# Performance work log

Hardware: AMD Instinct MI355X
Metric: run time of the kernel (lower is better)

The kernel has to match this reference:

```python
import jax, jax.numpy as jnp
import numpy as np

N = 50000   # nodes
E = 800000  # edges
F = 128     # feat_dim
LN_EPS = 1e-5


def setup_inputs() -> dict:
    key = jax.random.key(0)
    ks = jax.random.split(key, 16)

    def lin(k, fan_in, shape):
        # roughly kaiming-uniform-like scale; exact init is irrelevant for correctness
        return jax.random.normal(k, shape, jnp.float32) * (1.0 / np.sqrt(fan_in))

    inp = {
        "x": jax.random.normal(ks[0], (N, F), jnp.float32),
        "pos": jax.random.normal(ks[1], (N, 3), jnp.float32),
        "edge_index": jax.random.randint(ks[2], (2, E), 0, N, jnp.int64),
        # edge_mlp: Linear(2F+1 -> F), SiLU, Linear(F -> F)
        "ew1": lin(ks[3], 2 * F + 1, (2 * F + 1, F)),
        "eb1": jnp.zeros((F,), jnp.float32),
        "ew2": lin(ks[4], F, (F, F)),
        "eb2": jnp.zeros((F,), jnp.float32),
        # node_mlp: Linear(F -> F), SiLU, Linear(F -> F)
        "nw1": lin(ks[5], F, (F, F)),
        "nb1": jnp.zeros((F,), jnp.float32),
        "nw2": lin(ks[6], F, (F, F)),
        "nb2": jnp.zeros((F,), jnp.float32),
        # coord_mlp: Linear(F -> 1), Tanh
        "cw": lin(ks[7], F, (F, 1)),
        "cb": jnp.zeros((1,), jnp.float32),
        # LayerNorm(F)
        "gamma": jnp.ones((F,), jnp.float32),
        "beta": jnp.zeros((F,), jnp.float32),
    }
    return inp


def reference(x, pos, edge_index, ew1, eb1, ew2, eb2, nw1, nb1, nw2, nb2, cw, cb, gamma, beta):
    row, col = edge_index[0], edge_index[1]

    diff = pos[row] - pos[col]                              # [E, 3]
    dist2 = jnp.sum(diff * diff, axis=1, keepdims=True)     # [E, 1]
    edge_feat = jnp.concatenate([x[row], x[col], dist2], axis=1)  # [E, 2F+1]

    # edge MLP (dropout p=0 -> identity in eval)
    msg = jax.nn.silu(edge_feat @ ew1 + eb1) @ ew2 + eb2    # [E, F]

    # scatter-add messages to source nodes
    agg = jax.ops.segment_sum(msg, row, num_segments=N)     # [N, F]

    # node MLP + residual + LayerNorm
    upd = jax.nn.silu(agg @ nw1 + nb1) @ nw2 + nb2          # [N, F]
    pre = x + upd
    mean = jnp.mean(pre, axis=-1, keepdims=True)
    var = jnp.mean(jnp.square(pre - mean), axis=-1, keepdims=True)
    x_out = gamma * (pre - mean) * jax.lax.rsqrt(var + LN_EPS) + beta

    # coordinate update
    scale = jnp.tanh(msg @ cw + cb)                         # [E, 1]
    delta = jax.ops.segment_sum(scale * diff, row, num_segments=N)  # [N, 3]
    pos_out = pos + delta
    return (x_out, pos_out)
```

## Files before the change

### kernel.cpp

```cpp
#include <hip/hip_runtime.h>
#include <math.h>

#define NN 50000
#define EE 800000
#define FF 128

constexpr float LN_EPS = 1e-5f;
constexpr int NC = (NN + 255) / 256;

typedef float  f32x4  __attribute__((ext_vector_type(4)));
typedef short  s16x8  __attribute__((ext_vector_type(8)));

__device__ __forceinline__ float silu_f(float v) {
    return v / (1.f + __expf(-v));
}

__device__ __forceinline__ unsigned short f2bf(float f) {
    union { float f; unsigned u; } cv; cv.f = f;
    unsigned u = cv.u;
    u += 0x7fffu + ((u >> 16) & 1u);
    return (unsigned short)(u >> 16);
}

__device__ __forceinline__ float bf2f(unsigned short u) {
    union { unsigned u; float f; } cv; cv.u = ((unsigned)u) << 16;
    return cv.f;
}

__global__ __launch_bounds__(256) void convert_x_kernel(
    const float* __restrict__ x, unsigned short* __restrict__ xb)
{
    int i = (blockIdx.x * 256 + threadIdx.x) * 8;
    float4 a = *(const float4*)&x[i];
    float4 b = *(const float4*)&x[i + 4];
    s16x8 o;
    o[0] = (short)f2bf(a.x); o[1] = (short)f2bf(a.y);
    o[2] = (short)f2bf(a.z); o[3] = (short)f2bf(a.w);
    o[4] = (short)f2bf(b.x); o[5] = (short)f2bf(b.y);
    o[6] = (short)f2bf(b.z); o[7] = (short)f2bf(b.w);
    *(s16x8*)&xb[i] = o;
}

__global__ __launch_bounds__(256) void transpose_w_kernel(
    const float* __restrict__ ew1, const float* __restrict__ ew2,
    const float* __restrict__ nw1, const float* __restrict__ nw2,
    unsigned short* __restrict__ ew1T, unsigned short* __restrict__ ew2T,
    unsigned short* __restrict__ nw1T, unsigned short* __restrict__ nw2T)
{
    int o = blockIdx.x * 256 + threadIdx.x;
    if (o < 32768) {
        int n = o >> 8, k = o & 255;
        ew1T[o] = f2bf(ew1[k * FF + n]);
    } else if (o < 49152) {
        int o2 = o - 32768; int n = o2 >> 7, k = o2 & 127;
        ew2T[o2] = f2bf(ew2[k * FF + n]);
    } else if (o < 65536) {
        int o2 = o - 49152; int n = o2 >> 7, k = o2 & 127;
        nw1T[o2] = f2bf(nw1[k * FF + n]);
    } else {
        int o2 = o - 65536; int n = o2 >> 7, k = o2 & 127;
        nw2T[o2] = f2bf(nw2[k * FF + n]);
    }
}

__global__ __launch_bounds__(256) void hist_kernel(
    const int* __restrict__ ei, int* __restrict__ cnt)
{
    int e = blockIdx.x * 256 + threadIdx.x;
    if (e < EE) atomicAdd(&cnt[ei[e]], 1);
}

__global__ __launch_bounds__(256) void chunk_sum_kernel(
    const int* __restrict__ cnt, int* __restrict__ chunkSum)
{
    __shared__ int s[256];
    int t = threadIdx.x;
    int idx = blockIdx.x * 256 + t;
    s[t] = (idx < NN) ? cnt[idx] : 0;
    __syncthreads();
    for (int off = 128; off > 0; off >>= 1) {
        if (t < off) s[t] += s[t + off];
        __syncthreads();
    }
    if (t == 0) chunkSum[blockIdx.x] = s[0];
}

__global__ __launch_bounds__(256) void scan_chunks_kernel(
    const int* __restrict__ chunkSum, int* __restrict__ chunkOff)
{
    __shared__ int s[256];
    int t = threadIdx.x;
    int v = (t < NC) ? chunkSum[t] : 0;
    s[t] = v;
    __syncthreads();
    for (int off = 1; off < 256; off <<= 1) {
        int u = (t >= off) ? s[t - off] : 0;
        __syncthreads();
        s[t] += u;
        __syncthreads();
    }
    if (t < NC) chunkOff[t] = s[t] - v;
}

__global__ __launch_bounds__(256) void scan_kernel(
    const int* __restrict__ cnt, const int* __restrict__ chunkOff,
    int* __restrict__ offs, int* __restrict__ rowStart)
{
    __shared__ int s[256];
    int t = threadIdx.x;
    int idx = blockIdx.x * 256 + t;
    int v = (idx < NN) ? cnt[idx] : 0;
    s[t] = v;
    __syncthreads();
    for (int off = 1; off < 256; off <<= 1) {
        int u = (t >= off) ? s[t - off] : 0;
        __syncthreads();
        s[t] += u;
        __syncthreads();
    }
    if (idx < NN) {
        int st = chunkOff[blockIdx.x] + s[t] - v;
        offs[idx] = st;
        rowStart[idx] = st;
    }
}

__global__ __launch_bounds__(256) void scatter_idx_kernel(
    const int* __restrict__ ei, int* __restrict__ offs,
    int* __restrict__ sRow, int* __restrict__ sCol)
{
    int e = blockIdx.x * 256 + threadIdx.x;
    if (e < EE) {
        int r = ei[e], c = ei[EE + e];
        int p = atomicAdd(&offs[r], 1);
        sRow[p] = r;
        sCol[p] = c;
    }
}

constexpr int EPB   = 64;
constexpr int NTILE = EE / EPB;
constexpr int XAS   = 264;
constexpr int H1S   = 136;

__global__ __launch_bounds__(512, 4) void edgeA_kernel(
    const unsigned short* __restrict__ xb, const float* __restrict__ pos,
    const int* __restrict__ sRow, const int* __restrict__ sCol,
    const unsigned short* __restrict__ ew1T, const float* __restrict__ ew1,
    const float* __restrict__ eb1,
    const unsigned short* __restrict__ ew2T, const float* __restrict__ eb2,
    const float* __restrict__ cw,  const float* __restrict__ cb,
    unsigned short* __restrict__ msgb, float* __restrict__ sSg)
{
    __shared__ float dist2S[EPB];
    __shared__ float sPart[8][EPB];
    __shared__ __align__(16) unsigned short xa  [EPB * XAS];
    __shared__ __align__(16) unsigned short h1  [EPB * H1S];
    __shared__ __align__(16) unsigned short msgL[EPB * H1S];

    const int t   = threadIdx.x;
    const int w   = t >> 6;
    const int l   = t & 63;
    const int l15 = l & 15;
    const int q8  = l >> 4;
    const int n   = w * 16 + l15;

    s16x8 B1[8], B2[4];
    #pragma unroll
    for (int ko = 0; ko < 8; ++ko)
        B1[ko] = *(const s16x8*)(ew1T + (size_t)n * 256 + ko * 32 + q8 * 8);
    #pragma unroll
    for (int ko = 0; ko < 4; ++ko)
        B2[ko] = *(const s16x8*)(ew2T + (size_t)n * 128 + ko * 32 + q8 * 8);
    const float w256 = ew1[256 * FF + n];
    const float b1   = eb1[n];
    const float b2   = eb2[n];
    const float cwc  = cw[n];
    const float cb0  = cb[0];

    const int q   = t & 31;
    const int eB  = t >> 5;
    const int ksel = (q & 15) * 8;
    const int* idxBase = (q < 16) ? sRow : sCol;

    int   nidx[4];
    s16x8 ag[4];
    {
        int e0 = blockIdx.x * EPB;
        #pragma unroll
        for (int i = 0; i < 4; ++i) nidx[i] = idxBase[e0 + eB + 16 * i];
        #pragma unroll
        for (int i = 0; i < 4; ++i) ag[i] = *(const s16x8*)(xb + (size_t)nidx[i] * FF + ksel);
    }

    for (int tile = blockIdx.x; tile < NTILE; tile += gridDim.x) {
        const int e0 = tile * EPB;

        #pragma unroll
        for (int i = 0; i < 4; ++i)
            *(s16x8*)(xa + (eB + 16 * i) * XAS + q * 8) = ag[i];
        if (t < EPB) {
            int r = sRow[e0 + t];
            int c = sCol[e0 + t];
            float dx = pos[r*3+0] - pos[c*3+0];
            float dy = pos[r*3+1] - pos[c*3+1];
            float dz = pos[r*3+2] - pos[c*3+2];
            dist2S[t] = dx*dx + dy*dy + dz*dz;
        }
        __syncthreads();

        {
            int tn  = tile + gridDim.x;
            int e0n = (tn < NTILE) ? tn * EPB : 0;
            #pragma unroll
            for (int i = 0; i < 4; ++i) nidx[i] = idxBase[e0n + eB + 16 * i];
            #pragma unroll
            for (int i = 0; i < 4; ++i) ag[i] = *(const s16x8*)(xb + (size_t)nidx[i] * FF + ksel);
        }

        f32x4 acc[4] = {};
        #pragma unroll
        for (int mt = 0; mt < 4; ++mt) {
            const unsigned short* ar = xa + (mt * 16 + l15) * XAS + q8 * 8;
            #pragma unroll
            for (int ko = 0; ko < 8; ++ko) {
                s16x8 a = *(const s16x8*)(ar + ko * 32);
                acc[mt] = __builtin_amdgcn_mfma_f32_16x16x32_bf16(a, B1[ko], acc[mt], 0, 0, 0);
            }
        }

        #pragma unroll
        for (int mt = 0; mt < 4; ++mt) {
            #pragma unroll
            for (int r = 0; r < 4; ++r) {
                int e = mt * 16 + q8 * 4 + r;
                float v = acc[mt][r] + dist2S[e] * w256 + b1;
                h1[e * H1S + n] = f2bf(silu_f(v));
            }
        }
        __syncthreads();

        f32x4 acc2[4] = {};
        #pragma unroll
        for (int mt = 0; mt < 4; ++mt) {
            const unsigned short* hr = h1 + (mt * 16 + l15) * H1S + q8 * 8;
            #pragma unroll
            for (int ko = 0; ko < 4; ++ko) {
                s16x8 a = *(const s16x8*)(hr + ko * 32);
                acc2[mt] = __builtin_amdgcn_mfma_f32_16x16x32_bf16(a, B2[ko], acc2[mt], 0, 0, 0);
            }
        }

        #pragma unroll
        for (int mt = 0; mt < 4; ++mt) {
            #pragma unroll
            for (int r = 0; r < 4; ++r) {
                float m = acc2[mt][r] + b2;
                float p = m * cwc;
                p += __shfl_xor(p, 1);
                p += __shfl_xor(p, 2);
                p += __shfl_xor(p, 4);
                p += __shfl_xor(p, 8);
                int e = mt * 16 + q8 * 4 + r;
                if (l15 == 0) sPart[w][e] = p;
                msgL[e * H1S + n] = f2bf(m);
            }
        }
        __syncthreads();

        if (t < EPB) {
            float p = 0.f;
            #pragma unroll
            for (int ww = 0; ww < 8; ++ww) p += sPart[ww][t];
            sSg[e0 + t] = tanhf(p + cb0);
        }

        #pragma unroll
        for (int i = 0; i < 2; ++i) {
            int idx = i * 512 + t;
            int e   = idx >> 4;
            int c   = idx & 15;
            *(s16x8*)&msgb[(size_t)(e0 + e) * FF + c * 8] =
                *(const s16x8*)&msgL[e * H1S + c * 8];
        }
    }
}

constexpr int NPB  = 16;
constexpr int ABS  = 136;

__global__ __launch_bounds__(128) void nodeB_kernel(
    const float* __restrict__ x, const float* __restrict__ pos,
    const unsigned short* __restrict__ msgb, const float* __restrict__ sSg,
    const int* __restrict__ sCol, const int* __restrict__ rowStart,
    const unsigned short* __restrict__ nw1T, const float* __restrict__ nb1,
    const unsigned short* __restrict__ nw2T, const float* __restrict__ nb2,
    const float* __restrict__ gamma, const float* __restrict__ beta,
    float* __restrict__ xout, float* __restrict__ posout)
{
    __shared__ __align__(16) unsigned short aB [NPB * ABS];
    __shared__ __align__(16) unsigned short h1B[NPB * ABS];
    __shared__ float sRedS[2][NPB];
    __shared__ float sRedQ[2][NPB];

    const int t   = threadIdx.x;
    const int w   = t >> 6;
    const int l   = t & 63;
    const int l15 = l & 15;
    const int q8  = l >> 4;

    const int n0 = blockIdx.x * NPB;

    for (int e = 0; e < NPB; ++e) {
        int nn = n0 + e;
        int p0 = rowStart[nn];
        int p1 = (nn == NN - 1) ? EE : rowStart[nn + 1];
        float s0 = 0.f, s1 = 0.f, s2 = 0.f, s3 = 0.f;
        int p = p0;
        for (; p + 4 <= p1; p += 4) {
            s0 += bf2f(msgb[(size_t)(p    ) * FF + t]);
            s1 += bf2f(msgb[(size_t)(p + 1) * FF + t]);
            s2 += bf2f(msgb[(size_t)(p + 2) * FF + t]);
            s3 += bf2f(msgb[(size_t)(p + 3) * FF + t]);
        }
        for (; p < p1; ++p) s0 += bf2f(msgb[(size_t)p * FF + t]);
        aB[e * ABS + t] = f2bf((s0 + s1) + (s2 + s3));
    }

    if (t < NPB * 3) {
        int e = t / 3, d = t % 3;
        int nn = n0 + e;
        int p0 = rowStart[nn];
        int p1 = (nn == NN - 1) ? EE : rowStart[nn + 1];
        float pn = pos[nn * 3 + d];
        float sum = 0.f;
        for (int p = p0; p < p1; ++p) {
            int c = sCol[p];
            sum += sSg[p] * (pn - pos[c * 3 + d]);
        }
        posout[nn * 3 + d] = pn + sum;
    }
    __syncthreads();

    int ncol[4];
    #pragma unroll
    for (int tt = 0; tt < 4; ++tt) ncol[tt] = w * 64 + tt * 16 + l15;

    f32x4 acc[4] = {};
    {
        const unsigned short* ar = aB + l15 * ABS + q8 * 8;
        #pragma unroll
        for (int ko = 0; ko < 4; ++ko) {
            s16x8 a = *(const s16x8*)(ar + ko * 32);
            #pragma unroll
            for (int tt = 0; tt < 4; ++tt) {
                s16x8 b = *(const s16x8*)(nw1T + (size_t)ncol[tt] * 128 + ko * 32 + q8 * 8);
                acc[tt] = __builtin_amdgcn_mfma_f32_16x16x32_bf16(a, b, acc[tt], 0, 0, 0);
            }
        }
    }
    #pragma unroll
    for (int tt = 0; tt < 4; ++tt) {
        float bb = nb1[ncol[tt]];
        #pragma unroll
        for (int r = 0; r < 4; ++r) {
            int e = q8 * 4 + r;
            h1B[e * ABS + ncol[tt]] = f2bf(silu_f(acc[tt][r] + bb));
        }
    }
    __syncthreads();

    f32x4 acc2[4] = {};
    {
        const unsigned short* hr = h1B + l15 * ABS + q8 * 8;
        #pragma unroll
        for (int ko = 0; ko < 4; ++ko) {
            s16x8 a = *(const s16x8*)(hr + ko * 32);
            #pragma unroll
            for (int tt = 0; tt < 4; ++tt) {
                s16x8 b = *(const s16x8*)(nw2T + (size_t)ncol[tt] * 128 + ko * 32 + q8 * 8);
                acc2[tt] = __builtin_amdgcn_mfma_f32_16x16x32_bf16(a, b, acc2[tt], 0, 0, 0);
            }
        }
    }

    float pre[4][4];
    #pragma unroll
    for (int tt = 0; tt < 4; ++tt) {
        float bb = nb2[ncol[tt]];
        #pragma unroll
        for (int r = 0; r < 4; ++r) {
            int e = q8 * 4 + r;
            pre[tt][r] = x[(size_t)(n0 + e) * FF + ncol[tt]] + acc2[tt][r] + bb;
        }
    }
    #pragma unroll
    for (int r = 0; r < 4; ++r) {
        float s = 0.f, sq = 0.f;
        #pragma unroll
        for (int tt = 0; tt < 4; ++tt) {
            s  += pre[tt][r];
            sq += pre[tt][r] * pre[tt][r];
        }
        s  += __shfl_xor(s, 1);  sq += __shfl_xor(sq, 1);
        s  += __shfl_xor(s, 2);  sq += __shfl_xor(sq, 2);
        s  += __shfl_xor(s, 4);  sq += __shfl_xor(sq, 4);
        s  += __shfl_xor(s, 8);  sq += __shfl_xor(sq, 8);
        if (l15 == 0) {
            int e = q8 * 4 + r;
            sRedS[w][e] = s;
            sRedQ[w][e] = sq;
        }
    }
    __syncthreads();

    #pragma unroll
    for (int tt = 0; tt < 4; ++tt) {
        float g = gamma[ncol[tt]], bb = beta[ncol[tt]];
        #pragma unroll
        for (int r = 0; r < 4; ++r) {
            int e = q8 * 4 + r;
            float mean = (sRedS[0][e] + sRedS[1][e]) * (1.f / FF);
            float m2   = (sRedQ[0][e] + sRedQ[1][e]) * (1.f / FF);
            float var  = m2 - mean * mean;
            float xo   = g * (pre[tt][r] - mean) * rsqrtf(var + LN_EPS) + bb;
            xout[(size_t)(n0 + e) * FF + ncol[tt]] = xo;
        }
    }
}

extern "C" void kernel_launch(void* const* d_in, const int* in_sizes, int n_in,
                              void* d_out, int out_size, void* d_ws, size_t ws_size,
                              hipStream_t stream) {
    const float* x    = (const float*)d_in[0];
    const float* pos  = (const float*)d_in[1];
    const int*   ei   = (const int*)  d_in[2];
    const float* ew1  = (const float*)d_in[3];
    const float* eb1  = (const float*)d_in[4];
    const float* ew2  = (const float*)d_in[5];
    const float* eb2  = (const float*)d_in[6];
    const float* nw1  = (const float*)d_in[7];
    const float* nb1  = (const float*)d_in[8];
    const float* nw2  = (const float*)d_in[9];
    const float* nb2  = (const float*)d_in[10];
    const float* cw   = (const float*)d_in[11];
    const float* cb   = (const float*)d_in[12];
    const float* gam  = (const float*)d_in[13];
    const float* bet  = (const float*)d_in[14];

    float* out    = (float*)d_out;
    float* xout   = out;
    float* posout = out + (size_t)NN * FF;

    auto align256 = [](size_t v) { return (v + 255) & ~(size_t)255; };
    char* ws = (char*)d_ws;

    size_t CNT_B   = align256((size_t)NN * 4);
    size_t OFFS_B  = align256((size_t)NN * 4);
    size_t RST_B   = align256((size_t)NN * 4);
    size_t CHNK_B  = align256((size_t)NC * 4 * 2);
    size_t SROW_B  = align256((size_t)EE * 4);
    size_t XB_B    = align256((size_t)NN * FF * 2);
    size_t EW1T_B  = align256((size_t)128 * 256 * 2);
    size_t WT_B    = align256((size_t)128 * 128 * 2);
    size_t MSGB_B  = align256((size_t)EE * FF * 2);

    size_t o = 0;
    int* cnt       = (int*)(ws + o);  o += CNT_B;
    int* offs      = (int*)(ws + o);  o += OFFS_B;
    int* rowStart  = (int*)(ws + o);  o += RST_B;
    int* chunkSum  = (int*)(ws + o);
    int* chunkOff  = chunkSum + NC;   o += CHNK_B;
    int* sRow      = (int*)(ws + o);  o += SROW_B;
    int* sCol      = (int*)(ws + o);  o += SROW_B;
    unsigned short* xb   = (unsigned short*)(ws + o);  o += XB_B;
    unsigned short* ew1T = (unsigned short*)(ws + o);  o += EW1T_B;
    unsigned short* ew2T = (unsigned short*)(ws + o);  o += WT_B;
    unsigned short* nw1T = (unsigned short*)(ws + o);  o += WT_B;
    unsigned short* nw2T = (unsigned short*)(ws + o);  o += WT_B;
    unsigned short* msgb = (unsigned short*)(ws + o);  o += MSGB_B;
    float*          sSg  = (float*)(ws + o);

    hipMemsetAsync(cnt, 0, CNT_B, stream);

    convert_x_kernel<<<(NN * FF / 8) / 256, 256, 0, stream>>>(x, xb);
    transpose_w_kernel<<<(32768 + 3 * 16384) / 256, 256, 0, stream>>>(
        ew1, ew2, nw1, nw2, ew1T, ew2T, nw1T, nw2T);

    hist_kernel<<<(EE + 255) / 256, 256, 0, stream>>>(ei, cnt);
    chunk_sum_kernel<<<NC, 256, 0, stream>>>(cnt, chunkSum);
    scan_chunks_kernel<<<1, 256, 0, stream>>>(chunkSum, chunkOff);
    scan_kernel<<<NC, 256, 0, stream>>>(cnt, chunkOff, offs, rowStart);
    scatter_idx_kernel<<<(EE + 255) / 256, 256, 0, stream>>>(ei, offs, sRow, sCol);

    edgeA_kernel<<<2048, 512, 0, stream>>>(
        xb, pos, sRow, sCol, ew1T, ew1, eb1, ew2T, eb2, cw, cb, msgb, sSg);

    nodeB_kernel<<<NN / NPB, 128, 0, stream>>>(
        x, pos, msgb, sSg, sCol, rowStart,
        nw1T, nb1, nw2T, nb2, gam, bet, xout, posout);
}
```

Before: 527.6 us.

## Widen node kernel to 512 threads with vectorized per-wave segment aggregation

The node kernel grows from 128 to 512 threads per block. Each of the 8 waves now aggregates two nodes' message rows using 16-byte bf16 vector loads, with four edges in flight per wave and a shuffle reduction, replacing the serial per-node loop that loaded one element per thread. The node MLPs are re-split so each wave owns one 16-column MFMA tile instead of four, and the LayerNorm partial sums are reduced across 8 waves. This aims to raise memory-level parallelism in the gather-heavy aggregation, at the cost of larger blocks and more cross-wave reduction.

```diff
diff --git a/kernel.cpp b/kernel.cpp
--- a/kernel.cpp
+++ b/kernel.cpp
@@ -286,10 +286,10 @@
     }
 }
 
-constexpr int NPB  = 16;
-constexpr int ABS  = 136;
-
-__global__ __launch_bounds__(128) void nodeB_kernel(
+constexpr int NPB = 16;
+constexpr int ABS = 136;
+
+__global__ __launch_bounds__(512) void nodeB_kernel(
     const float* __restrict__ x, const float* __restrict__ pos,
     const unsigned short* __restrict__ msgb, const float* __restrict__ sSg,
     const int* __restrict__ sCol, const int* __restrict__ rowStart,
@@ -300,31 +300,51 @@
 {
     __shared__ __align__(16) unsigned short aB [NPB * ABS];
     __shared__ __align__(16) unsigned short h1B[NPB * ABS];
-    __shared__ float sRedS[2][NPB];
-    __shared__ float sRedQ[2][NPB];
+    __shared__ float sRedS[8][NPB];
+    __shared__ float sRedQ[8][NPB];
 
     const int t   = threadIdx.x;
     const int w   = t >> 6;
     const int l   = t & 63;
     const int l15 = l & 15;
     const int q8  = l >> 4;
-
-    const int n0 = blockIdx.x * NPB;
-
-    for (int e = 0; e < NPB; ++e) {
+    const int n0  = blockIdx.x * NPB;
+    const int n   = w * 16 + l15;
+
+    #pragma unroll
+    for (int s = 0; s < 2; ++s) {
+        int e  = 2 * w + s;
         int nn = n0 + e;
         int p0 = rowStart[nn];
         int p1 = (nn == NN - 1) ? EE : rowStart[nn + 1];
-        float s0 = 0.f, s1 = 0.f, s2 = 0.f, s3 = 0.f;
-        int p = p0;
-        for (; p + 4 <= p1; p += 4) {
-            s0 += bf2f(msgb[(size_t)(p    ) * FF + t]);
-            s1 += bf2f(msgb[(size_t)(p + 1) * FF + t]);
-            s2 += bf2f(msgb[(size_t)(p + 2) * FF + t]);
-            s3 += bf2f(msgb[(size_t)(p + 3) * FF + t]);
-        }
-        for (; p < p1; ++p) s0 += bf2f(msgb[(size_t)p * FF + t]);
-        aB[e * ABS + t] = f2bf((s0 + s1) + (s2 + s3));
+        float a0=0.f,a1=0.f,a2=0.f,a3=0.f,a4=0.f,a5=0.f,a6=0.f,a7=0.f;
+        for (int p = p0 + q8; p < p1; p += 4) {
+            s16x8 v = *(const s16x8*)(msgb + (size_t)p * FF + l15 * 8);
+            a0 += bf2f((unsigned short)v[0]);
+            a1 += bf2f((unsigned short)v[1]);
+            a2 += bf2f((unsigned short)v[2]);
+            a3 += bf2f((unsigned short)v[3]);
+            a4 += bf2f((unsigned short)v[4]);
+            a5 += bf2f((unsigned short)v[5]);
+            a6 += bf2f((unsigned short)v[6]);
+            a7 += bf2f((unsigned short)v[7]);
+        }
+        a0 += __shfl_xor(a0,16); a1 += __shfl_xor(a1,16);
+        a2 += __shfl_xor(a2,16); a3 += __shfl_xor(a3,16);
+        a4 += __shfl_xor(a4,16); a5 += __shfl_xor(a5,16);
+        a6 += __shfl_xor(a6,16); a7 += __shfl_xor(a7,16);
+        a0 += __shfl_xor(a0,32); a1 += __shfl_xor(a1,32);
+        a2 += __shfl_xor(a2,32); a3 += __shfl_xor(a3,32);
+        a4 += __shfl_xor(a4,32); a5 += __shfl_xor(a5,32);
+        a6 += __shfl_xor(a6,32); a7 += __shfl_xor(a7,32);
+        if (q8 == 0) {
+            s16x8 o;
+            o[0]=(short)f2bf(a0); o[1]=(short)f2bf(a1);
+            o[2]=(short)f2bf(a2); o[3]=(short)f2bf(a3);
+            o[4]=(short)f2bf(a4); o[5]=(short)f2bf(a5);
+            o[6]=(short)f2bf(a6); o[7]=(short)f2bf(a7);
+            *(s16x8*)(aB + e * ABS + l15 * 8) = o;
+        }
     }
 
     if (t < NPB * 3) {
@@ -342,70 +362,53 @@
     }
     __syncthreads();
 
-    int ncol[4];
-    #pragma unroll
-    for (int tt = 0; tt < 4; ++tt) ncol[tt] = w * 64 + tt * 16 + l15;
-
-    f32x4 acc[4] = {};
+    f32x4 acc = {};
     {
         const unsigned short* ar = aB + l15 * ABS + q8 * 8;
         #pragma unroll
         for (int ko = 0; ko < 4; ++ko) {
             s16x8 a = *(const s16x8*)(ar + ko * 32);
-            #pragma unroll
-            for (int tt = 0; tt < 4; ++tt) {
-                s16x8 b = *(const s16x8*)(nw1T + (size_t)ncol[tt] * 128 + ko * 32 + q8 * 8);
-                acc[tt] = __builtin_amdgcn_mfma_f32_16x16x32_bf16(a, b, acc[tt], 0, 0, 0);
-            }
-        }
-    }
-    #pragma unroll
-    for (int tt = 0; tt < 4; ++tt) {
-        float bb = nb1[ncol[tt]];
+            s16x8 b = *(const s16x8*)(nw1T + (size_t)n * 128 + ko * 32 + q8 * 8);
+            acc = __builtin_amdgcn_mfma_f32_16x16x32_bf16(a, b, acc, 0, 0, 0);
+        }
+    }
+    {
+        float bb = nb1[n];
         #pragma unroll
         for (int r = 0; r < 4; ++r) {
             int e = q8 * 4 + r;
-            h1B[e * ABS + ncol[tt]] = f2bf(silu_f(acc[tt][r] + bb));
+            h1B[e * ABS + n] = f2bf(silu_f(acc[r] + bb));
         }
     }
     __syncthreads();
 
-    f32x4 acc2[4] = {};
+    f32x4 acc2 = {};
     {
         const unsigned short* hr = h1B + l15 * ABS + q8 * 8;
         #pragma unroll
         for (int ko = 0; ko < 4; ++ko) {
             s16x8 a = *(const s16x8*)(hr + ko * 32);
-            #pragma unroll
-            for (int tt = 0; tt < 4; ++tt) {
-                s16x8 b = *(const s16x8*)(nw2T + (size_t)ncol[tt] * 128 + ko * 32 + q8 * 8);
-                acc2[tt] = __builtin_amdgcn_mfma_f32_16x16x32_bf16(a, b, acc2[tt], 0, 0, 0);
-            }
-        }
-    }
-
-    float pre[4][4];
-    #pragma unroll
-    for (int tt = 0; tt < 4; ++tt) {
-        float bb = nb2[ncol[tt]];
+            s16x8 b = *(const s16x8*)(nw2T + (size_t)n * 128 + ko * 32 + q8 * 8);
+            acc2 = __builtin_amdgcn_mfma_f32_16x16x32_bf16(a, b, acc2, 0, 0, 0);
+        }
+    }
+
+    float pre[4];
+    {
+        float bb = nb2[n];
         #pragma unroll
         for (int r = 0; r < 4; ++r) {
             int e = q8 * 4 + r;
-            pre[tt][r] = x[(size_t)(n0 + e) * FF + ncol[tt]] + acc2[tt][r] + bb;
+            pre[r] = x[(size_t)(n0 + e) * FF + n] + acc2[r] + bb;
         }
     }
     #pragma unroll
     for (int r = 0; r < 4; ++r) {
-        float s = 0.f, sq = 0.f;
-        #pragma unroll
-        for (int tt = 0; tt < 4; ++tt) {
-            s  += pre[tt][r];
-            sq += pre[tt][r] * pre[tt][r];
-        }
-        s  += __shfl_xor(s, 1);  sq += __shfl_xor(sq, 1);
-        s  += __shfl_xor(s, 2);  sq += __shfl_xor(sq, 2);
-        s  += __shfl_xor(s, 4);  sq += __shfl_xor(sq, 4);
-        s  += __shfl_xor(s, 8);  sq += __shfl_xor(sq, 8);
+        float s = pre[r], sq = pre[r] * pre[r];
+        s += __shfl_xor(s, 1);  sq += __shfl_xor(sq, 1);
+        s += __shfl_xor(s, 2);  sq += __shfl_xor(sq, 2);
+        s += __shfl_xor(s, 4);  sq += __shfl_xor(sq, 4);
+        s += __shfl_xor(s, 8);  sq += __shfl_xor(sq, 8);
         if (l15 == 0) {
             int e = q8 * 4 + r;
             sRedS[w][e] = s;
@@ -414,17 +417,18 @@
     }
     __syncthreads();
 
-    #pragma unroll
-    for (int tt = 0; tt < 4; ++tt) {
-        float g = gamma[ncol[tt]], bb = beta[ncol[tt]];
+    {
+        float g = gamma[n], bt = beta[n];
         #pragma unroll
         for (int r = 0; r < 4; ++r) {
             int e = q8 * 4 + r;
-            float mean = (sRedS[0][e] + sRedS[1][e]) * (1.f / FF);
-            float m2   = (sRedQ[0][e] + sRedQ[1][e]) * (1.f / FF);
-            float var  = m2 - mean * mean;
-            float xo   = g * (pre[tt][r] - mean) * rsqrtf(var + LN_EPS) + bb;
-            xout[(size_t)(n0 + e) * FF + ncol[tt]] = xo;
+            float S = 0.f, Q = 0.f;
+            #pragma unroll
+            for (int ww = 0; ww < 8; ++ww) { S += sRedS[ww][e]; Q += sRedQ[ww][e]; }
+            float mean = S * (1.f / FF);
+            float var  = Q * (1.f / FF) - mean * mean;
+            xout[(size_t)(n0 + e) * FF + n] =
+                g * (pre[r] - mean) * rsqrtf(var + LN_EPS) + bt;
         }
     }
 }
@@ -496,7 +500,7 @@
     edgeA_kernel<<<2048, 512, 0, stream>>>(
         xb, pos, sRow, sCol, ew1T, ew1, eb1, ew2T, eb2, cw, cb, msgb, sSg);
 
-    nodeB_kernel<<<NN / NPB, 128, 0, stream>>>(
+    nodeB_kernel<<<NN / NPB, 512, 0, stream>>>(
         x, pos, msgb, sSg, sCol, rowStart,
         nw1T, nb1, nw2T, nb2, gam, bet, xout, posout);
 }
```

Result: faster. 517.0 us (-2.0%).
